# Performance work log

Measured on AMD Instinct MI355X. Metric: run time of the kernel, lower is better.

Reference implementation:

```python
import jax, jax.numpy as jnp
import numpy as np
import math

# Model dims (see init_kwargs)
B_SZ, L, D_MODEL = 1, 2048, 512
H, G, P, N, R = 16, 4, 64, 32, 2
RATIO = H // G
CHUNK = 256
EPS = 1e-5
DIM_Z = H * P
DIM_X = H * P
DIM_B = G * N * R
DIM_C = G * N * R
D_PROJ = DIM_Z + DIM_X + DIM_B + DIM_C + G + G


def setup_inputs() -> dict:
    key = jax.random.key(0)
    ks = jax.random.split(key, 8)
    u = jax.random.normal(ks[0], (B_SZ, L, D_MODEL), jnp.float32)
    W_in = jax.random.normal(ks[1], (D_PROJ, D_MODEL), jnp.float32) * (1.0 / math.sqrt(D_MODEL))
    b_in = np.zeros(D_PROJ, np.float32)
    # dt bias init: inverse softplus of dt ~ LogUniform(dt_min, dt_max)
    dt0 = np.exp(np.random.RandomState(0).rand(G) * (math.log(0.1) - math.log(0.001)) + math.log(0.001))
    inv_dt = dt0 + np.log(-np.expm1(-dt0))
    s = DIM_Z + DIM_X + DIM_B + DIM_C
    b_in[s:s + G] = inv_dt
    b_in[s + G:] = -3.0  # lambda bias
    b_in = jnp.asarray(b_in)
    W_xup = jax.random.normal(ks[2], (P * R, P), jnp.float32) * (1.0 / math.sqrt(P * R))
    W_ydown = jax.random.normal(ks[3], (P, P * R), jnp.float32) * (1.0 / math.sqrt(P * R))
    A_log = jnp.log(jax.random.uniform(ks[4], (G,), jnp.float32, 1.0, 16.0))
    theta_log = jax.random.normal(ks[5], (G, N // 2), jnp.float32)
    D = jnp.ones((H,), jnp.float32)
    norm_B_w = jnp.ones((N * R,), jnp.float32)
    norm_C_w = jnp.ones((N * R,), jnp.float32)
    bias_B = jnp.ones((G, N, R), jnp.float32)
    bias_C = jnp.ones((G, N, R), jnp.float32)
    W_out = jax.random.normal(ks[6], (D_MODEL, H * P), jnp.float32) * (1.0 / math.sqrt(H * P))
    return dict(u=u, W_in=W_in, b_in=b_in, W_xup=W_xup, W_ydown=W_ydown,
                A_log=A_log, theta_log=theta_log, D=D,
                norm_B_w=norm_B_w, norm_C_w=norm_C_w,
                bias_B=bias_B, bias_C=bias_C, W_out=W_out)


def _rms(x, w):
    return x * jax.lax.rsqrt(jnp.mean(x * x, axis=-1, keepdims=True) + EPS) * w


def _rope(x, ang):
    # x: (B,L,H,N,R), ang: (B,L,H,N/2) -- rotate interleaved (real,imag) pairs along N
    sh = x.shape
    xr = x.reshape(sh[:-2] + (N // 2, 2, R))
    re, im = xr[..., 0, :], xr[..., 1, :]
    c = jnp.cos(ang)[..., None]
    s = jnp.sin(ang)[..., None]
    out = jnp.stack([re * c - im * s, re * s + im * c], axis=-2)
    return out.reshape(sh)


def _chunk_scan(u, dt, A, C, cs):
    # u: (B,L,H,N,P), dt: (B,L,H), A: (H,), C: (B,L,H,N,R). L % cs == 0.
    B, Ltot, Hh, Nn, Pp = u.shape
    Rr = C.shape[-1]
    nc = Ltot // cs
    la = (dt * A).reshape(B, nc, cs, Hh)                      # log decay per step
    uc = u.reshape(B, nc, cs, Hh, Nn, Pp)
    Cc = C.reshape(B, nc, cs, Hh, Nn, Rr)
    # intra-chunk pairwise decay matrix (stable segsum)
    lap = la.transpose(0, 1, 3, 2)                            # (B,nc,H,cs)
    cums = jnp.cumsum(lap, axis=-1)
    seg = cums[..., :, None] - cums[..., None, :]
    mask = jnp.tril(jnp.ones((cs, cs), bool))
    Lmask = jnp.where(mask, jnp.exp(seg), 0.0)                # (B,nc,H,cs,cs)
    h_intra = jnp.einsum('bchij,bcjhnp->bcihnp', Lmask, uc)   # (B,nc,cs,H,N,P)
    y_diag = jnp.einsum('bclhnp,bclhnr->bclhpr', h_intra, Cc)
    decay_chunk = jnp.exp(jnp.sum(la, axis=2))                # (B,nc,H)
    h_last = h_intra[:, :, -1]                                # (B,nc,H,N,P)
    # inter-chunk sequential scan (state at the START of each chunk)
    def step(h, inp):
        d, cl = inp
        return h * d[:, :, None, None] + cl, h
    h0 = jnp.zeros((B, Hh, Nn, Pp), u.dtype)
    hF, h_states = jax.lax.scan(step, h0, (decay_chunk.transpose(1, 0, 2), h_last.transpose(1, 0, 2, 3, 4)))
    h_states = h_states.transpose(1, 0, 2, 3, 4)              # (B,nc,H,N,P)
    decay_intra = jnp.exp(jnp.cumsum(la, axis=2))             # (B,nc,cs,H)
    h_eff = jnp.einsum('bchnp,bclh->bclhnp', h_states, decay_intra)
    y_off = jnp.einsum('bclhnp,bclhnr->bclhpr', h_eff, Cc)
    y = (y_diag + y_off).reshape(B, Ltot, Hh, Pp, Rr)
    return y, hF


def reference(u, W_in, b_in, W_xup, W_ydown, A_log, theta_log, D,
              norm_B_w, norm_C_w, bias_B, bias_C, W_out):
    B_sz = u.shape[0]
    proj = u @ W_in.T + b_in                                  # (B,L,D_PROJ)
    s0, s1, s2, s3, s4 = DIM_Z, DIM_Z + DIM_X, DIM_Z + DIM_X + DIM_B, DIM_Z + DIM_X + DIM_B + DIM_C, DIM_Z + DIM_X + DIM_B + DIM_C + G
    z = proj[..., :s0]
    xp = proj[..., s0:s1].reshape(B_sz, L, H, P)
    Bp = proj[..., s1:s2]
    Cp = proj[..., s2:s3]
    dt = proj[..., s3:s4]                                     # (B,L,G)
    lam = proj[..., s4:]                                      # (B,L,G)
    xp = jax.nn.silu(xp)
    dt = jax.nn.softplus(dt)
    A = -jnp.exp(A_log)                                       # (G,)
    theta = jnp.exp(theta_log)                                # (G,N/2)
    # broadcast groups -> heads
    dt_h = jnp.repeat(dt, RATIO, axis=2)                      # (B,L,H)
    A_h = jnp.repeat(A, RATIO)                                # (H,)
    theta_h = jnp.repeat(theta, RATIO, axis=0)                # (H,N/2)
    lam_h = jax.nn.sigmoid(jnp.repeat(lam, RATIO, axis=2))    # (B,L,H)
    # data-dependent RoPE angles: cumulative dt*theta
    dt_theta = jnp.einsum('blh,hn->blhn', dt_h, theta_h)
    angles = jnp.cumsum(dt_theta, axis=1)                     # (B,L,H,N/2)
    # B / C: RMSNorm over N*R, add bias, broadcast groups, rotate
    Bp = _rms(Bp.reshape(B_sz, L, G, N * R), norm_B_w).reshape(B_sz, L, G, N, R) + bias_B
    Cp = _rms(Cp.reshape(B_sz, L, G, N * R), norm_C_w).reshape(B_sz, L, G, N, R) + bias_C
    B_rot = _rope(jnp.repeat(Bp, RATIO, axis=2), -angles)     # (B,L,H,N,R)
    C_rot = _rope(jnp.repeat(Cp, RATIO, axis=2), angles)
    # MIMO up projection
    x_up = (xp @ W_xup.T).reshape(B_sz, L, H, P, R)
    u_in = jnp.einsum('blhnr,blhpr->blhnp', B_rot, x_up) * dt_h[..., None, None]
    # generalized trapezoidal rule: mix current and decayed previous input
    alpha = jnp.exp(dt_h * A_h)                               # (B,L,H)
    u_prev = jnp.pad(u_in[:, :-1], ((0, 0), (1, 0), (0, 0), (0, 0), (0, 0)))
    u_eff = (1.0 - lam_h)[..., None, None] * u_in + (lam_h * alpha)[..., None, None] * u_prev
    y, _ = _chunk_scan(u_eff, dt_h, A_h, C_rot, CHUNK)        # (B,L,H,P,R)
    # MIMO down projection + D skip + gate
    y = y.reshape(B_sz, L, H, P * R) @ W_ydown.T              # (B,L,H,P)
    y = y + D[None, None, :, None] * xp
    y = y * jax.nn.silu(z.reshape(B_sz, L, H, P))
    out = y.reshape(B_sz, L, H * P) @ W_out.T
    return out
```

## Files before the change

### kernel.cpp

```cpp
#include <hip/hip_runtime.h>
#include <hip/hip_bf16.h>
#include <math.h>

namespace {

typedef unsigned short u16;
typedef __bf16 bf16x8 __attribute__((ext_vector_type(8)));
typedef float f32x4 __attribute__((ext_vector_type(4)));

constexpr int L_SEQ  = 2048;
constexpr int DPROJ  = 2568;
constexpr int OFF_X  = 1024;
constexpr int OFF_B  = 2048;
constexpr int OFF_C  = 2304;
constexpr int OFF_DT = 2560;
constexpr int SCHUNK = 16;
constexpr int NCH    = L_SEQ / SCHUNK;

__device__ inline u16 f2bf(float x) {
  unsigned u = __float_as_uint(x);
  unsigned r = u + 0x7FFFu + ((u >> 16) & 1u);
  return (u16)(r >> 16);
}
__device__ inline float bf2f(u16 h) {
  return __uint_as_float(((unsigned)h) << 16);
}

__device__ inline void split_body(const float* __restrict__ src, int rows,
                                  int cols, int stride, int idx,
                                  u16* __restrict__ hi, u16* __restrict__ lo)
{
  int c4cnt = cols >> 2;
  int row = idx / c4cnt;
  int c4  = (idx % c4cnt) << 2;
  float4 v = make_float4(0.f, 0.f, 0.f, 0.f);
  if (row < rows) v = *(const float4*)(src + (size_t)row * stride + c4);
  float x[4] = {v.x, v.y, v.z, v.w};
  u16 h[4], l[4];
#pragma unroll
  for (int j = 0; j < 4; ++j) {
    h[j] = f2bf(x[j]);
    l[j] = f2bf(x[j] - bf2f(h[j]));
  }
  size_t off = (size_t)row * cols + c4;
  *(ushort4*)(hi + off) = make_ushort4(h[0], h[1], h[2], h[3]);
  *(ushort4*)(lo + off) = make_ushort4(l[0], l[1], l[2], l[3]);
}

__global__ __launch_bounds__(256)
void convert_all(const float* __restrict__ W_in, const float* __restrict__ W_xup,
                 const float* __restrict__ W_ydown, const float* __restrict__ W_out,
                 const float* __restrict__ u,
                 u16* __restrict__ win_hi, u16* __restrict__ win_lo,
                 u16* __restrict__ wxup_hi, u16* __restrict__ wxup_lo,
                 u16* __restrict__ wyd_hi, u16* __restrict__ wyd_lo,
                 u16* __restrict__ wout_hi, u16* __restrict__ wout_lo,
                 u16* __restrict__ u_hi, u16* __restrict__ u_lo)
{
  int b = blockIdx.x;
  if (b < 1344) {
    split_body(W_in, 2568, 512, 512, b * 256 + threadIdx.x, win_hi, win_lo);
  } else if (b < 1352) {
    split_body(W_xup, 128, 64, 64, (b - 1344) * 256 + threadIdx.x, wxup_hi, wxup_lo);
  } else if (b < 1360) {
    split_body(W_ydown, 64, 128, 128, (b - 1352) * 256 + threadIdx.x, wyd_hi, wyd_lo);
  } else if (b < 1872) {
    split_body(W_out, 512, 1024, 1024, (b - 1360) * 256 + threadIdx.x, wout_hi, wout_lo);
  } else {
    split_body(u, 2048, 512, 512, (b - 1872) * 256 + threadIdx.x, u_hi, u_lo);
  }
}

__device__ inline void gload16(const u16* g, u16* l) {
  __builtin_amdgcn_global_load_lds(
      (const __attribute__((address_space(1))) unsigned int*)g,
      (__attribute__((address_space(3))) unsigned int*)l, 16, 0, 0);
}

__device__ inline void xcd_swizzle(int& bx, int& by, int& bz) {
  int nx = gridDim.x, ny = gridDim.y;
  int nwg = nx * ny * gridDim.z;
  int flat = blockIdx.x + nx * (blockIdx.y + ny * blockIdx.z);
  int cpx = nwg >> 3;
  int swz = (flat & 7) * cpx + (flat >> 3);
  bx = swz % nx;
  int r = swz / nx;
  by = r % ny;
  bz = r / ny;
}

template<int WMW, int WNW, bool GATE>
__global__ __launch_bounds__(64 * WMW * WNW)
void gemm_mfma(const u16* __restrict__ Ah, const u16* __restrict__ Al,
               const u16* __restrict__ Bh, const u16* __restrict__ Bl,
               const float* __restrict__ bias,
               float* __restrict__ C, int ldc, int N,
               int Kstride, int Klen, size_t c_slice,
               const float* __restrict__ Dv,
               const u16* __restrict__ xs_hi, const u16* __restrict__ xs_lo,
               const float* __restrict__ projz,
               u16* __restrict__ yg_hi, u16* __restrict__ yg_lo)
{
  constexpr int BM = 64 * WMW, BN = 64 * WNW;
  constexpr int WAVES = WMW * WNW;
  constexpr int RG_A = BM / 16, RG_B = BN / 16;
  constexpr int NG = 2 * RG_A + 2 * RG_B;
  constexpr int GPW = NG / WAVES;
  static_assert(NG % WAVES == 0, "");

  __shared__ u16 sAB[2][NG * 512];

  int bx, by, bz;
  xcd_swizzle(bx, by, bz);

  const int tid  = threadIdx.x;
  const int wave = tid >> 6;
  const int lane = tid & 63;
  const int wm   = wave % WMW;
  const int wn   = wave / WMW;
  const int bm   = bx * BM;
  const int bn   = by * BN;
  const int koff = bz * Klen;
  const int lrow = lane & 15;
  const int lkc  = lane >> 4;
  const int sr   = lane >> 2;
  const int sk8  = (lane & 3) * 8;

  const u16* gptr[GPW];
#pragma unroll
  for (int t = 0; t < GPW; ++t) {
    int g = wave * GPW + t;
    const u16* base;
    int rowbase;
    if (g < 2 * RG_A) {
      int hl = g / RG_A, i = g % RG_A;
      base = hl ? Al : Ah;  rowbase = bm + i * 16;
    } else {
      int g2 = g - 2 * RG_A;
      int hl = g2 / RG_B, i = g2 % RG_B;
      base = hl ? Bl : Bh;  rowbase = bn + i * 16;
    }
    gptr[t] = base + (size_t)(rowbase + sr) * Kstride + koff + sk8;
  }

  f32x4 acc[4][4];
#pragma unroll
  for (int i = 0; i < 4; ++i)
#pragma unroll
    for (int j = 0; j < 4; ++j) acc[i][j] = (f32x4){0.f, 0.f, 0.f, 0.f};

#define STAGE(b, kk)                                             \
  {                                                              \
    _Pragma("unroll")                                            \
    for (int t = 0; t < GPW; ++t)                                \
      gload16(gptr[t] + (kk), &sAB[b][(wave * GPW + t) * 512]);  \
  }

  STAGE(0, 0);
  asm volatile("s_waitcnt vmcnt(0)" ::: "memory");
  __syncthreads();

  int buf = 0;
  for (int k0 = 0; k0 < Klen; k0 += 32) {
    if (k0 + 32 < Klen) STAGE(buf ^ 1, k0 + 32);

    const u16* sb = sAB[buf];
    bf16x8 a_h[4], a_l[4], b_h[4], b_l[4];
#pragma unroll
    for (int i = 0; i < 4; ++i) {
      a_h[i] = *(const bf16x8*)&sb[(0 * RG_A + wm * 4 + i) * 512 + lrow * 32 + lkc * 8];
      a_l[i] = *(const bf16x8*)&sb[(1 * RG_A + wm * 4 + i) * 512 + lrow * 32 + lkc * 8];
      b_h[i] = *(const bf16x8*)&sb[(2 * RG_A + 0 * RG_B + wn * 4 + i) * 512 + lrow * 32 + lkc * 8];
      b_l[i] = *(const bf16x8*)&sb[(2 * RG_A + 1 * RG_B + wn * 4 + i) * 512 + lrow * 32 + lkc * 8];
    }
#pragma unroll
    for (int i = 0; i < 4; ++i)
#pragma unroll
      for (int j = 0; j < 4; ++j) {
        acc[i][j] = __builtin_amdgcn_mfma_f32_16x16x32_bf16(a_h[i], b_h[j], acc[i][j], 0, 0, 0);
        acc[i][j] = __builtin_amdgcn_mfma_f32_16x16x32_bf16(a_l[i], b_h[j], acc[i][j], 0, 0, 0);
        acc[i][j] = __builtin_amdgcn_mfma_f32_16x16x32_bf16(a_h[i], b_l[j], acc[i][j], 0, 0, 0);
      }

    asm volatile("s_waitcnt vmcnt(0)" ::: "memory");
    __syncthreads();
    buf ^= 1;
  }
#undef STAGE

  const int r0 = (lane >> 4) * 4;
  if (!GATE) {
    float* Cs = C + (size_t)bz * c_slice;
#pragma unroll
    for (int j = 0; j < 4; ++j) {
      int col = bn + wn * 64 + j * 16 + lrow;
      if (col >= N) continue;
      float bv = bias ? bias[col] : 0.f;
#pragma unroll
      for (int i = 0; i < 4; ++i) {
        int rowb = bm + wm * 64 + i * 16 + r0;
#pragma unroll
        for (int r = 0; r < 4; ++r)
          Cs[(size_t)(rowb + r) * ldc + col] = acc[i][j][r] + bv;
      }
    }
  } else {
#pragma unroll
    for (int j = 0; j < 4; ++j) {
      int col = bn + wn * 64 + j * 16 + lrow;
#pragma unroll
      for (int i = 0; i < 4; ++i) {
        int rowb = bm + wm * 64 + i * 16 + r0;
#pragma unroll
        for (int r = 0; r < 4; ++r) {
          int row = rowb + r;
          int l = row >> 4, h = row & 15;
          size_t ei = (size_t)l * 1024 + (h << 6) + col;
          float xsv = bf2f(xs_hi[ei]) + bf2f(xs_lo[ei]);
          float z = projz[(size_t)l * DPROJ + (h << 6) + col];
          float v = (acc[i][j][r] + Dv[h] * xsv) * (z / (1.f + expf(-z)));
          u16 hh = f2bf(v);
          yg_hi[ei] = hh;
          yg_lo[ei] = f2bf(v - bf2f(hh));
        }
      }
    }
  }
}

__global__ __launch_bounds__(256)
void reduce4_kernel(const float* __restrict__ p, float* __restrict__ o)
{
  const int n = L_SEQ * 512 / 4;
  int i = blockIdx.x * 256 + threadIdx.x;
  if (i >= n) return;
  float4 a = ((const float4*)p)[i];
  float4 b = ((const float4*)p)[i + n];
  float4 c = ((const float4*)p)[i + 2 * n];
  float4 d = ((const float4*)p)[i + 3 * n];
  float4 r;
  r.x = (a.x + b.x) + (c.x + d.x);
  r.y = (a.y + b.y) + (c.y + d.y);
  r.z = (a.z + b.z) + (c.z + d.z);
  r.w = (a.w + b.w) + (c.w + d.w);
  ((float4*)o)[i] = r;
}

__global__ __launch_bounds__(256)
void dtlam_kernel(const float* __restrict__ u, const float* __restrict__ W_in,
                  const float* __restrict__ b_in, const float* __restrict__ A_log,
                  float* __restrict__ dtg, float* __restrict__ alphag,
                  float* __restrict__ c0g, float* __restrict__ c1g)
{
  int tid  = blockIdx.x * 256 + threadIdx.x;
  int pair = tid >> 4;
  int ln   = tid & 15;
  int l = pair >> 2, g = pair & 3;
  const float4* ur = (const float4*)(u + (size_t)l * 512) + ln * 8;
  const float4* wd = (const float4*)(W_in + (size_t)(OFF_DT + g) * 512) + ln * 8;
  const float4* wl = (const float4*)(W_in + (size_t)(OFF_DT + 4 + g) * 512) + ln * 8;
  float sd = 0.f, sl = 0.f;
#pragma unroll
  for (int k = 0; k < 8; ++k) {
    float4 a = ur[k], b = wd[k], c = wl[k];
    sd += a.x * b.x + a.y * b.y + a.z * b.z + a.w * b.w;
    sl += a.x * c.x + a.y * c.y + a.z * c.z + a.w * c.w;
  }
#pragma unroll
  for (int m = 1; m < 16; m <<= 1) {
    sd += __shfl_xor(sd, m, 64);
    sl += __shfl_xor(sl, m, 64);
  }
  if (ln == 0) {
    sd += b_in[OFF_DT + g];
    sl += b_in[OFF_DT + 4 + g];
    float dt  = (sd > 20.f) ? sd : log1pf(expf(sd));
    float lam = 1.f / (1.f + expf(-sl));
    float Ag  = -expf(A_log[g]);
    float al  = expf(dt * Ag);
    dtg[pair]    = dt;
    alphag[pair] = al;
    c0g[pair]    = 1.f - lam;
    c1g[pair]    = lam * al;
  }
}

__global__ __launch_bounds__(256)
void cumsum_dt_kernel(const float* __restrict__ dtg,
                      const float* __restrict__ theta_log,
                      float* __restrict__ cumdt, float* __restrict__ angred)
{
  const int g = blockIdx.x;
  const int t = threadIdx.x;
  constexpr int PER = L_SEQ / 256;
  __shared__ double ps[256];
  double th[16];
#pragma unroll
  for (int f = 0; f < 16; ++f) th[f] = exp((double)theta_log[g * 16 + f]);
  float loc[PER];
  double s = 0.0;
  int l0 = t * PER;
  for (int i = 0; i < PER; ++i) {
    loc[i] = dtg[(l0 + i) * 4 + g];
    s += (double)loc[i];
  }
  ps[t] = s;
  __syncthreads();
  for (int off = 1; off < 256; off <<= 1) {
    double v = (t >= off) ? ps[t - off] : 0.0;
    __syncthreads();
    ps[t] += v;
    __syncthreads();
  }
  double c = ps[t] - s;
  const double inv2pi = 0.15915494309189535;
  const double twopi  = 6.283185307179586;
  for (int i = 0; i < PER; ++i) {
    c += (double)loc[i];
    cumdt[(l0 + i) * 4 + g] = (float)c;
#pragma unroll
    for (int f = 0; f < 16; ++f) {
      double rev = th[f] * c * inv2pi;
      double fr  = rev - floor(rev);
      angred[(size_t)(l0 + i) * 64 + g * 16 + f] = (float)(fr * twopi);
    }
  }
}

__global__ __launch_bounds__(256)
void pertoken_kernel(const float* __restrict__ proj,
                     const float* __restrict__ angred,
                     const float* __restrict__ norm_B_w,
                     const float* __restrict__ norm_C_w,
                     const float* __restrict__ bias_B,
                     const float* __restrict__ bias_C,
                     u16* __restrict__ xs_hi, u16* __restrict__ xs_lo,
                     float* __restrict__ Brot,
                     float* __restrict__ Crot)
{
  const int l = blockIdx.x;
  const int t = threadIdx.x;
  const size_t prow = (size_t)l * DPROJ;

  for (int i = t; i < 1024; i += 256) {
    float x = proj[prow + OFF_X + i];
    float s = x / (1.f + expf(-x));
    u16 hh = f2bf(s);
    xs_hi[(size_t)l * 1024 + i] = hh;
    xs_lo[(size_t)l * 1024 + i] = f2bf(s - bf2f(hh));
  }

  const int g = t >> 6;
  const int e = t & 63;
  float bv = proj[prow + OFF_B + t];
  float cv = proj[prow + OFF_C + t];
  float ssb = bv * bv, ssc = cv * cv;
#pragma unroll
  for (int m = 1; m <= 32; m <<= 1) {
    ssb += __shfl_xor(ssb, m, 64);
    ssc += __shfl_xor(ssc, m, 64);
  }
  float nb = bv * rsqrtf(ssb * (1.f / 64.f) + 1e-5f) * norm_B_w[e] + bias_B[t];
  float nc = cv * rsqrtf(ssc * (1.f / 64.f) + 1e-5f) * norm_C_w[e] + bias_C[t];

  float ang = angred[(size_t)l * 64 + g * 16 + (e >> 2)];
  float ca, sa;
  sincosf(ang, &sa, &ca);
  float nb2 = __shfl_xor(nb, 2, 64);
  float nc2 = __shfl_xor(nc, 2, 64);
  bool isre = ((e >> 1) & 1) == 0;
  float Bo, Co;
  if (isre) {
    Bo = nb * ca + nb2 * sa;
    Co = nc * ca - nc2 * sa;
  } else {
    Bo = nb * ca - nb2 * sa;
    Co = nc * ca + nc2 * sa;
  }
  Brot[(size_t)l * 256 + t] = Bo;
  Crot[(size_t)l * 256 + t] = Co;
}

template<bool WITH_Y>
__global__ __launch_bounds__(256)
void scan_chunk(const float* __restrict__ Brot, const float* __restrict__ Crot,
                const float* __restrict__ xup,
                const float* __restrict__ dtg, const float* __restrict__ alphag,
                const float* __restrict__ c0g, const float* __restrict__ c1g,
                const float* __restrict__ hstates_in,
                float* __restrict__ hlast_out,
                u16* __restrict__ yhi, u16* __restrict__ ylo)
{
  const int c   = blockIdx.x;
  const int g   = blockIdx.y;
  const int wid = threadIdx.x >> 6;
  const int p   = threadIdx.x & 63;
  const int h   = g * 4 + wid;
  const int l0  = c * SCHUNK;

  __shared__ float Bs[SCHUNK][64];
  __shared__ float Cs[SCHUNK][64];
  __shared__ float als[SCHUNK], c0s[SCHUNK], c1s[SCHUNK];

  for (int i = threadIdx.x; i < SCHUNK * 64; i += 256) {
    int l = i >> 6, e = i & 63;
    float dt = dtg[(l0 + l) * 4 + g];
    Bs[l][e] = dt * Brot[(size_t)(l0 + l) * 256 + g * 64 + e];
    if (WITH_Y) Cs[l][e] = Crot[(size_t)(l0 + l) * 256 + g * 64 + e];
  }
  if (threadIdx.x < SCHUNK) {
    int l = threadIdx.x;
    als[l] = alphag[(l0 + l) * 4 + g];
    c0s[l] = c0g[(l0 + l) * 4 + g];
    c1s[l] = c1g[(l0 + l) * 4 + g];
  }
  __syncthreads();

  float H[32], up[32];
  if (WITH_Y) {
    const float* hs = &hstates_in[(((size_t)c * 16 + h) * 64 + p) * 32];
#pragma unroll
    for (int q = 0; q < 8; ++q) {
      float4 v = *reinterpret_cast<const float4*>(hs + 4 * q);
      H[4 * q] = v.x; H[4 * q + 1] = v.y; H[4 * q + 2] = v.z; H[4 * q + 3] = v.w;
    }
  } else {
#pragma unroll
    for (int n = 0; n < 32; ++n) H[n] = 0.f;
  }

  if (c > 0) {
    const int lm = l0 - 1;
    const float dtm = dtg[lm * 4 + g];
    float2 X = *reinterpret_cast<const float2*>(&xup[((size_t)lm * 16 + h) * 128 + 2 * p]);
    float x0 = dtm * X.x, x1 = dtm * X.y;
#pragma unroll
    for (int n = 0; n < 32; ++n) {
      float2 Bv = *reinterpret_cast<const float2*>(&Brot[(size_t)lm * 256 + g * 64 + 2 * n]);
      up[n] = Bv.x * x0 + Bv.y * x1;
    }
  } else {
#pragma unroll
    for (int n = 0; n < 32; ++n) up[n] = 0.f;
  }

  for (int l = 0; l < SCHUNK; ++l) {
    float2 X = *reinterpret_cast<const float2*>(
        &xup[((size_t)(l0 + l) * 16 + h) * 128 + 2 * p]);
    const float al = als[l], cc0 = c0s[l], cc1 = c1s[l];
    float y0 = 0.f, y1 = 0.f;
#pragma unroll
    for (int n2 = 0; n2 < 16; ++n2) {
      float4 Bv = *reinterpret_cast<const float4*>(&Bs[l][4 * n2]);
      float uin0 = Bv.x * X.x + Bv.y * X.y;
      float uin1 = Bv.z * X.x + Bv.w * X.y;
      float ue0 = cc0 * uin0 + cc1 * up[2 * n2];
      float ue1 = cc0 * uin1 + cc1 * up[2 * n2 + 1];
      H[2 * n2]     = al * H[2 * n2]     + ue0;
      H[2 * n2 + 1] = al * H[2 * n2 + 1] + ue1;
      up[2 * n2] = uin0; up[2 * n2 + 1] = uin1;
      if (WITH_Y) {
        float4 Cv = *reinterpret_cast<const float4*>(&Cs[l][4 * n2]);
        y0 = fmaf(H[2 * n2], Cv.x, fmaf(H[2 * n2 + 1], Cv.z, y0));
        y1 = fmaf(H[2 * n2], Cv.y, fmaf(H[2 * n2 + 1], Cv.w, y1));
      }
    }
    if (WITH_Y) {
      size_t ofs = ((size_t)(l0 + l) * 16 + h) * 128 + 2 * p;
      u16 h0 = f2bf(y0), h1 = f2bf(y1);
      *(ushort2*)&yhi[ofs] = make_ushort2(h0, h1);
      *(ushort2*)&ylo[ofs] = make_ushort2(f2bf(y0 - bf2f(h0)), f2bf(y1 - bf2f(h1)));
    }
  }

  if (!WITH_Y) {
    float* hl = &hlast_out[(((size_t)c * 16 + h) * 64 + p) * 32];
#pragma unroll
    for (int q = 0; q < 8; ++q)
      *reinterpret_cast<float4*>(hl + 4 * q) =
          make_float4(H[4 * q], H[4 * q + 1], H[4 * q + 2], H[4 * q + 3]);
  }
}

__global__ __launch_bounds__(256)
void scan_passB(const float* __restrict__ hlast, const float* __restrict__ cumdt,
                const float* __restrict__ A_log, float* __restrict__ hstates)
{
  int idx = blockIdx.x * 256 + threadIdx.x;
  int h = idx >> 11;
  int rem = idx & 2047;
  int g = h >> 2;
  float Ag = -expf(A_log[g]);
  float s = 0.f;
  for (int c0 = 0; c0 < NCH; c0 += 8) {
    float hlv[8], dec[8];
#pragma unroll
    for (int j = 0; j < 8; ++j) {
      int c = c0 + j;
      hlv[j] = hlast[((size_t)c * 16 + h) * 2048 + rem];
      float sd = cumdt[(c * SCHUNK + SCHUNK - 1) * 4 + g]
               - (c > 0 ? cumdt[(c * SCHUNK - 1) * 4 + g] : 0.f);
      dec[j] = expf(Ag * sd);
    }
#pragma unroll
    for (int j = 0; j < 8; ++j) {
      hstates[((size_t)(c0 + j) * 16 + h) * 2048 + rem] = s;
      s = fmaf(s, dec[j], hlv[j]);
    }
  }
}

}

extern "C" void kernel_launch(void* const* d_in, const int* in_sizes, int n_in,
                              void* d_out, int out_size, void* d_ws, size_t ws_size,
                              hipStream_t stream)
{
  const float* u         = (const float*)d_in[0];
  const float* W_in      = (const float*)d_in[1];
  const float* b_in      = (const float*)d_in[2];
  const float* W_xup     = (const float*)d_in[3];
  const float* W_ydown   = (const float*)d_in[4];
  const float* A_log     = (const float*)d_in[5];
  const float* theta_log = (const float*)d_in[6];
  const float* Dvec      = (const float*)d_in[7];
  const float* norm_B_w  = (const float*)d_in[8];
  const float* norm_C_w  = (const float*)d_in[9];
  const float* bias_B    = (const float*)d_in[10];
  const float* bias_C    = (const float*)d_in[11];
  const float* W_out     = (const float*)d_in[12];
  float* out = (float*)d_out;

  float* proj    = (float*)d_ws;
  float* xsreg   = proj    + (size_t)L_SEQ * DPROJ;
  float* dtg     = xsreg   + (size_t)L_SEQ * 1024;
  float* alphag  = dtg     + L_SEQ * 4;
  float* c0g     = alphag  + L_SEQ * 4;
  float* c1g     = c0g     + L_SEQ * 4;
  float* cumdt   = c1g     + L_SEQ * 4;
  float* angred  = cumdt   + L_SEQ * 4;
  float* Brot    = angred  + (size_t)L_SEQ * 64;
  float* Crot    = Brot    + (size_t)L_SEQ * 256;
  float* xup     = Crot    + (size_t)L_SEQ * 256;
  float* y128s   = xup     + (size_t)32768 * 128;
  float* rAf     = y128s   + (size_t)32768 * 128;
  float* hlast   = rAf     + (size_t)5100000;
  float* hstates = hlast   + (size_t)NCH * 16 * 2048;
  float* partials = y128s;

  u16* xs_hi = (u16*)xsreg;
  u16* xs_lo = xs_hi + (size_t)L_SEQ * 1024;
  u16* y128_hi = (u16*)y128s;
  u16* y128_lo = y128_hi + (size_t)32768 * 128;

  u16* rA = (u16*)rAf;
  u16* win_hi  = rA;
  u16* win_lo  = win_hi  + (size_t)2688 * 512;
  u16* wxup_hi = win_lo  + (size_t)2688 * 512;
  u16* wxup_lo = wxup_hi + (size_t)128 * 64;
  u16* wyd_hi  = wxup_lo + (size_t)128 * 64;
  u16* wyd_lo  = wyd_hi  + (size_t)64 * 128;
  u16* wout_hi = wyd_lo  + (size_t)64 * 128;
  u16* wout_lo = wout_hi + (size_t)512 * 1024;
  u16* u_hi    = wout_lo + (size_t)512 * 1024;
  u16* u_lo    = u_hi    + (size_t)2048 * 512;
  u16* yg_hi   = u_lo    + (size_t)2048 * 512;
  u16* yg_lo   = yg_hi   + (size_t)2048 * 1024;

  convert_all<<<dim3(2896), 256, 0, stream>>>(
      W_in, W_xup, W_ydown, W_out, u,
      win_hi, win_lo, wxup_hi, wxup_lo, wyd_hi, wyd_lo, wout_hi, wout_lo,
      u_hi, u_lo);
  gemm_mfma<2, 2, false><<<dim3(16, 21, 1), 256, 0, stream>>>(
      u_hi, u_lo, win_hi, win_lo, b_in, proj, DPROJ, DPROJ, 512, 512, 0,
      nullptr, nullptr, nullptr, nullptr, nullptr, nullptr);

  dtlam_kernel<<<dim3(512), 256, 0, stream>>>(u, W_in, b_in, A_log, dtg, alphag, c0g, c1g);
  cumsum_dt_kernel<<<dim3(4), 256, 0, stream>>>(dtg, theta_log, cumdt, angred);

  pertoken_kernel<<<dim3(L_SEQ), 256, 0, stream>>>(
      proj, angred, norm_B_w, norm_C_w, bias_B, bias_C,
      xs_hi, xs_lo, Brot, Crot);

  gemm_mfma<2, 2, false><<<dim3(256, 1, 1), 256, 0, stream>>>(
      xs_hi, xs_lo, wxup_hi, wxup_lo, nullptr, xup, 128, 128, 64, 64, 0,
      nullptr, nullptr, nullptr, nullptr, nullptr, nullptr);

  scan_chunk<false><<<dim3(NCH, 4), 256, 0, stream>>>(
      Brot, Crot, xup, dtg, alphag, c0g, c1g, nullptr, hlast, nullptr, nullptr);
  scan_passB<<<dim3(128), 256, 0, stream>>>(hlast, cumdt, A_log, hstates);
  scan_chunk<true><<<dim3(NCH, 4), 256, 0, stream>>>(
      Brot, Crot, xup, dtg, alphag, c0g, c1g, hstates, nullptr, y128_hi, y128_lo);

  gemm_mfma<2, 1, true><<<dim3(256, 1, 1), 128, 0, stream>>>(
      y128_hi, y128_lo, wyd_hi, wyd_lo, nullptr, nullptr, 0, 64, 128, 128, 0,
      Dvec, xs_hi, xs_lo, proj, yg_hi, yg_lo);

  gemm_mfma<2, 2, false><<<dim3(16, 4, 4), 256, 0, stream>>>(
      yg_hi, yg_lo, wout_hi, wout_lo, nullptr, partials, 512, 512, 1024, 256,
      (size_t)L_SEQ * 512,
      nullptr, nullptr, nullptr, nullptr, nullptr, nullptr);
  reduce4_kernel<<<dim3(1024), 256, 0, stream>>>(partials, out);
}
```

Before: 162.6 us.

## Fuse per-token SiLU, RMSNorm and RoPE into input projection GEMM epilogue

```diff
diff --git a/kernel.cpp b/kernel.cpp
--- a/kernel.cpp
+++ b/kernel.cpp
@@ -9,10 +9,6 @@
 typedef float f32x4 __attribute__((ext_vector_type(4)));
 
 constexpr int L_SEQ  = 2048;
-constexpr int DPROJ  = 2568;
-constexpr int OFF_X  = 1024;
-constexpr int OFF_B  = 2048;
-constexpr int OFF_C  = 2304;
 constexpr int OFF_DT = 2560;
 constexpr int SCHUNK = 16;
 constexpr int NCH    = L_SEQ / SCHUNK;
@@ -89,16 +85,20 @@
   bz = r / ny;
 }
 
-template<int WMW, int WNW, bool GATE>
+template<int WMW, int WNW, int EPI>
 __global__ __launch_bounds__(64 * WMW * WNW)
 void gemm_mfma(const u16* __restrict__ Ah, const u16* __restrict__ Al,
                const u16* __restrict__ Bh, const u16* __restrict__ Bl,
                const float* __restrict__ bias,
                float* __restrict__ C, int ldc, int N,
                int Kstride, int Klen, size_t c_slice,
+               const float* __restrict__ angred,
+               const float* __restrict__ norm_B_w, const float* __restrict__ norm_C_w,
+               const float* __restrict__ bias_B, const float* __restrict__ bias_C,
+               float* __restrict__ zbuf,
+               u16* __restrict__ xs_hi, u16* __restrict__ xs_lo,
+               float* __restrict__ Brot, float* __restrict__ Crot,
                const float* __restrict__ Dv,
-               const u16* __restrict__ xs_hi, const u16* __restrict__ xs_lo,
-               const float* __restrict__ projz,
                u16* __restrict__ yg_hi, u16* __restrict__ yg_lo)
 {
   constexpr int BM = 64 * WMW, BN = 64 * WNW;
@@ -189,7 +189,7 @@
 #undef STAGE
 
   const int r0 = (lane >> 4) * 4;
-  if (!GATE) {
+  if (EPI == 0) {
     float* Cs = C + (size_t)bz * c_slice;
 #pragma unroll
     for (int j = 0; j < 4; ++j) {
@@ -202,6 +202,94 @@
 #pragma unroll
         for (int r = 0; r < 4; ++r)
           Cs[(size_t)(rowb + r) * ldc + col] = acc[i][j][r] + bv;
+      }
+    }
+  } else if (EPI == 1) {
+    const int colbase = bn + wn * 64;
+    const int region  = colbase >> 6;
+    if (region >= 40) return;
+    if (region < 16) {
+#pragma unroll
+      for (int j = 0; j < 4; ++j) {
+        int col = colbase + j * 16 + lrow;
+        float bv = bias[col];
+#pragma unroll
+        for (int i = 0; i < 4; ++i) {
+          int rowb = bm + wm * 64 + i * 16 + r0;
+#pragma unroll
+          for (int r = 0; r < 4; ++r)
+            zbuf[(size_t)(rowb + r) * 1024 + col] = acc[i][j][r] + bv;
+        }
+      }
+    } else if (region < 32) {
+#pragma unroll
+      for (int j = 0; j < 4; ++j) {
+        int col = colbase + j * 16 + lrow;
+        float bv = bias[col];
+        int cx = col - 1024;
+#pragma unroll
+        for (int i = 0; i < 4; ++i) {
+          int rowb = bm + wm * 64 + i * 16 + r0;
+#pragma unroll
+          for (int r = 0; r < 4; ++r) {
+            float v = acc[i][j][r] + bv;
+            float s = v / (1.f + expf(-v));
+            u16 hh = f2bf(s);
+            size_t ei = (size_t)(rowb + r) * 1024 + cx;
+            xs_hi[ei] = hh;
+            xs_lo[ei] = f2bf(s - bf2f(hh));
+          }
+        }
+      }
+    } else {
+      const bool isB = region < 36;
+      const int  gg  = isB ? (region - 32) : (region - 36);
+      const float* nw  = isB ? norm_B_w : norm_C_w;
+      const float* bb  = isB ? bias_B : bias_C;
+      float* dst       = isB ? Brot : Crot;
+#pragma unroll
+      for (int i = 0; i < 4; ++i) {
+        const int rowb = bm + wm * 64 + i * 16 + r0;
+        float v[4][4];
+        float ss[4] = {0.f, 0.f, 0.f, 0.f};
+#pragma unroll
+        for (int j = 0; j < 4; ++j) {
+          int col = colbase + j * 16 + lrow;
+          float bv = bias[col];
+#pragma unroll
+          for (int r = 0; r < 4; ++r) {
+            v[j][r] = acc[i][j][r] + bv;
+            ss[r] = fmaf(v[j][r], v[j][r], ss[r]);
+          }
+        }
+#pragma unroll
+        for (int m = 1; m <= 8; m <<= 1)
+#pragma unroll
+          for (int r = 0; r < 4; ++r) ss[r] += __shfl_xor(ss[r], m, 64);
+        float rin[4];
+#pragma unroll
+        for (int r = 0; r < 4; ++r)
+          rin[r] = rsqrtf(ss[r] * (1.f / 64.f) + 1e-5f);
+#pragma unroll
+        for (int j = 0; j < 4; ++j) {
+          int e = j * 16 + lrow;
+          float w  = nw[e];
+          float b2 = bb[gg * 64 + e];
+          bool isre = ((e >> 1) & 1) == 0;
+#pragma unroll
+          for (int r = 0; r < 4; ++r) {
+            float nb = v[j][r] * rin[r] * w + b2;
+            float nb2 = __shfl_xor(nb, 2, 64);
+            int l = rowb + r;
+            float ang = angred[(size_t)l * 64 + gg * 16 + (e >> 2)];
+            float ca, sa;
+            sincosf(ang, &sa, &ca);
+            float o;
+            if (isB) o = isre ? (nb * ca + nb2 * sa) : (nb * ca - nb2 * sa);
+            else     o = isre ? (nb * ca - nb2 * sa) : (nb * ca + nb2 * sa);
+            dst[(size_t)l * 256 + gg * 64 + e] = o;
+          }
+        }
       }
     }
   } else {
@@ -217,7 +305,7 @@
           int l = row >> 4, h = row & 15;
           size_t ei = (size_t)l * 1024 + (h << 6) + col;
           float xsv = bf2f(xs_hi[ei]) + bf2f(xs_lo[ei]);
-          float z = projz[(size_t)l * DPROJ + (h << 6) + col];
+          float z = zbuf[ei];
           float v = (acc[i][j][r] + Dv[h] * xsv) * (z / (1.f + expf(-z)));
           u16 hh = f2bf(v);
           yg_hi[ei] = hh;
@@ -325,60 +413,6 @@
       angred[(size_t)(l0 + i) * 64 + g * 16 + f] = (float)(fr * twopi);
     }
   }
-}
-
-__global__ __launch_bounds__(256)
-void pertoken_kernel(const float* __restrict__ proj,
-                     const float* __restrict__ angred,
-                     const float* __restrict__ norm_B_w,
-                     const float* __restrict__ norm_C_w,
-                     const float* __restrict__ bias_B,
-                     const float* __restrict__ bias_C,
-                     u16* __restrict__ xs_hi, u16* __restrict__ xs_lo,
-                     float* __restrict__ Brot,
-                     float* __restrict__ Crot)
-{
-  const int l = blockIdx.x;
-  const int t = threadIdx.x;
-  const size_t prow = (size_t)l * DPROJ;
-
-  for (int i = t; i < 1024; i += 256) {
-    float x = proj[prow + OFF_X + i];
-    float s = x / (1.f + expf(-x));
-    u16 hh = f2bf(s);
-    xs_hi[(size_t)l * 1024 + i] = hh;
-    xs_lo[(size_t)l * 1024 + i] = f2bf(s - bf2f(hh));
-  }
-
-  const int g = t >> 6;
-  const int e = t & 63;
-  float bv = proj[prow + OFF_B + t];
-  float cv = proj[prow + OFF_C + t];
-  float ssb = bv * bv, ssc = cv * cv;
-#pragma unroll
-  for (int m = 1; m <= 32; m <<= 1) {
-    ssb += __shfl_xor(ssb, m, 64);
-    ssc += __shfl_xor(ssc, m, 64);
-  }
-  float nb = bv * rsqrtf(ssb * (1.f / 64.f) + 1e-5f) * norm_B_w[e] + bias_B[t];
-  float nc = cv * rsqrtf(ssc * (1.f / 64.f) + 1e-5f) * norm_C_w[e] + bias_C[t];
-
-  float ang = angred[(size_t)l * 64 + g * 16 + (e >> 2)];
-  float ca, sa;
-  sincosf(ang, &sa, &ca);
-  float nb2 = __shfl_xor(nb, 2, 64);
-  float nc2 = __shfl_xor(nc, 2, 64);
-  bool isre = ((e >> 1) & 1) == 0;
-  float Bo, Co;
-  if (isre) {
-    Bo = nb * ca + nb2 * sa;
-    Co = nc * ca - nc2 * sa;
-  } else {
-    Bo = nb * ca - nb2 * sa;
-    Co = nc * ca + nc2 * sa;
-  }
-  Brot[(size_t)l * 256 + t] = Bo;
-  Crot[(size_t)l * 256 + t] = Co;
 }
 
 template<bool WITH_Y>
@@ -531,8 +565,8 @@
   const float* W_out     = (const float*)d_in[12];
   float* out = (float*)d_out;
 
-  float* proj    = (float*)d_ws;
-  float* xsreg   = proj    + (size_t)L_SEQ * DPROJ;
+  float* zbuf    = (float*)d_ws;
+  float* xsreg   = zbuf    + (size_t)L_SEQ * 1024;
   float* dtg     = xsreg   + (size_t)L_SEQ * 1024;
   float* alphag  = dtg     + L_SEQ * 4;
   float* c0g     = alphag  + L_SEQ * 4;
@@ -571,20 +605,18 @@
       W_in, W_xup, W_ydown, W_out, u,
       win_hi, win_lo, wxup_hi, wxup_lo, wyd_hi, wyd_lo, wout_hi, wout_lo,
       u_hi, u_lo);
-  gemm_mfma<2, 2, false><<<dim3(16, 21, 1), 256, 0, stream>>>(
-      u_hi, u_lo, win_hi, win_lo, b_in, proj, DPROJ, DPROJ, 512, 512, 0,
-      nullptr, nullptr, nullptr, nullptr, nullptr, nullptr);
-
   dtlam_kernel<<<dim3(512), 256, 0, stream>>>(u, W_in, b_in, A_log, dtg, alphag, c0g, c1g);
   cumsum_dt_kernel<<<dim3(4), 256, 0, stream>>>(dtg, theta_log, cumdt, angred);
 
-  pertoken_kernel<<<dim3(L_SEQ), 256, 0, stream>>>(
-      proj, angred, norm_B_w, norm_C_w, bias_B, bias_C,
-      xs_hi, xs_lo, Brot, Crot);
-
-  gemm_mfma<2, 2, false><<<dim3(256, 1, 1), 256, 0, stream>>>(
+  gemm_mfma<2, 2, 1><<<dim3(16, 21, 1), 256, 0, stream>>>(
+      u_hi, u_lo, win_hi, win_lo, b_in, nullptr, 0, 2568, 512, 512, 0,
+      angred, norm_B_w, norm_C_w, bias_B, bias_C,
+      zbuf, xs_hi, xs_lo, Brot, Crot, nullptr, nullptr, nullptr);
+
+  gemm_mfma<2, 2, 0><<<dim3(256, 1, 1), 256, 0, stream>>>(
       xs_hi, xs_lo, wxup_hi, wxup_lo, nullptr, xup, 128, 128, 64, 64, 0,
-      nullptr, nullptr, nullptr, nullptr, nullptr, nullptr);
+      nullptr, nullptr, nullptr, nullptr, nullptr, nullptr, nullptr, nullptr,
+      nullptr, nullptr, nullptr, nullptr, nullptr);
 
   scan_chunk<false><<<dim3(NCH, 4), 256, 0, stream>>>(
       Brot, Crot, xup, dtg, alphag, c0g, c1g, nullptr, hlast, nullptr, nullptr);
@@ -592,13 +624,15 @@
   scan_chunk<true><<<dim3(NCH, 4), 256, 0, stream>>>(
       Brot, Crot, xup, dtg, alphag, c0g, c1g, hstates, nullptr, y128_hi, y128_lo);
 
-  gemm_mfma<2, 1, true><<<dim3(256, 1, 1), 128, 0, stream>>>(
+  gemm_mfma<2, 1, 2><<<dim3(256, 1, 1), 128, 0, stream>>>(
       y128_hi, y128_lo, wyd_hi, wyd_lo, nullptr, nullptr, 0, 64, 128, 128, 0,
-      Dvec, xs_hi, xs_lo, proj, yg_hi, yg_lo);
-
-  gemm_mfma<2, 2, false><<<dim3(16, 4, 4), 256, 0, stream>>>(
+      nullptr, nullptr, nullptr, nullptr, nullptr,
+      zbuf, xs_hi, xs_lo, nullptr, nullptr, Dvec, yg_hi, yg_lo);
+
+  gemm_mfma<2, 2, 0><<<dim3(16, 4, 4), 256, 0, stream>>>(
       yg_hi, yg_lo, wout_hi, wout_lo, nullptr, partials, 512, 512, 1024, 256,
       (size_t)L_SEQ * 512,
-      nullptr, nullptr, nullptr, nullptr, nullptr, nullptr);
+      nullptr, nullptr, nullptr, nullptr, nullptr, nullptr, nullptr, nullptr,
+      nullptr, nullptr, nullptr, nullptr, nullptr);
   reduce4_kernel<<<dim3(1024), 256, 0, stream>>>(partials, out);
 }
```

Result: slower. 233.6 us (+43.7%).
